# Kernel tuning notes

Hardware: AMD Instinct MI355X
Metric: run time of the kernel (lower is better)

## Reference

```python
import jax, jax.numpy as jnp
import numpy as np

N, E, C, NS, NB, NH = 20000, 320000, 64, 4, 8, 64
AVG_NEIGH = 16.0

def setup_inputs() -> dict:
    key = jax.random.key(0)
    ks = jax.random.split(key, 16)
    inp = {}
    inp['vectors'] = 0.35 * jax.random.normal(ks[0], (E, 3), jnp.float32)
    inp['node_scalars'] = jax.random.normal(ks[1], (N, C), jnp.float32)
    inp['node_vectors'] = jax.random.normal(ks[2], (N, C, 3), jnp.float32)
    inp['node_specie'] = jax.random.randint(ks[3], (N,), 0, NS)
    inp['senders'] = jax.random.randint(ks[4], (E,), 0, N)
    inp['receivers'] = jax.random.randint(ks[5], (E,), 0, N)
    # indexed skip linear: node irreps (64x0e+64x1o) -> 64x0e+64x1o+64x0e (scalars incl. gates)
    inp['W_skip_s'] = jax.random.normal(ks[6], (NS, C, 2 * C), jnp.float32) / np.sqrt(C)
    inp['W_skip_v'] = jax.random.normal(ks[7], (NS, C, C), jnp.float32) / np.sqrt(C)
    inp['W_up_s'] = jax.random.normal(ks[8], (C, C), jnp.float32) / np.sqrt(C)
    inp['W_up_v'] = jax.random.normal(ks[9], (C, C), jnp.float32) / np.sqrt(C)
    inp['W_mlp0'] = jax.random.normal(ks[10], (NB, NH), jnp.float32) / np.sqrt(NB)
    inp['W_mlp1'] = jax.random.normal(ks[11], (NH, NH), jnp.float32) / np.sqrt(NH)
    inp['W_mlp2'] = jax.random.normal(ks[12], (NH, 4 * C), jnp.float32) / np.sqrt(NH)
    inp['W_down_s'] = jax.random.normal(ks[13], (2 * C, 2 * C), jnp.float32) / np.sqrt(2 * C)
    inp['W_down_v'] = jax.random.normal(ks[14], (2 * C, C), jnp.float32) / np.sqrt(2 * C)
    return inp


def _forward(vectors, node_scalars, node_vectors, node_specie, senders, receivers,
             W_skip_s, W_skip_v, W_up_s, W_up_v, W_mlp0, W_mlp1, W_mlp2, W_down_s, W_down_v):
    n = node_scalars.shape[0]
    # --- self connection (specie-indexed linear) ---
    skip_s = jnp.einsum('ni,nio->no', node_scalars, W_skip_s[node_specie])   # [N,128]
    skip_v = jnp.einsum('nim,nio->nom', node_vectors, W_skip_v[node_specie]) # [N,64,3]
    # --- linear up ---
    s = node_scalars @ W_up_s                                  # [N,64]
    v = jnp.einsum('nim,io->nom', node_vectors, W_up_v)        # [N,64,3]
    ms, mv = s[senders], v[senders]                            # gather -> [E,64], [E,64,3]
    # --- spherical harmonics l=1, component normalization (|Y|=sqrt(3)) ---
    lengths = jnp.linalg.norm(vectors, axis=1, keepdims=True)  # [E,1]
    vhat = vectors / jnp.where(lengths == 0.0, 1.0, lengths)
    Y = jnp.sqrt(3.0) * vhat                                   # [E,3]
    # --- tensor product, filter_ir_out = {0e,1o} ---
    t1 = ms[:, :, None] * Y[:, None, :]                        # 0e x 1o -> 1o [E,64,3]
    t0 = jnp.einsum('ecm,em->ec', mv, Y) / jnp.sqrt(3.0)       # 1o x 1o -> 0e [E,64]
    msg_s = jnp.concatenate([ms, t0], axis=1)                  # [E,128]
    msg_v = jnp.concatenate([mv, t1], axis=1)                  # [E,128,3]
    # --- radial basis * polynomial envelope -> MLP ---
    x = lengths[:, 0]
    nvec = jnp.arange(1, NB + 1, dtype=vectors.dtype)
    safe_x = jnp.where(x == 0.0, 1.0, x)
    bess = jnp.sqrt(2.0) * jnp.sin(nvec * jnp.pi * x[:, None]) / safe_x[:, None]  # [E,8]
    u = jnp.clip(x, 0.0, 1.0)
    env = jnp.where(x < 1.0, 1.0 - 28.0 * u**6 + 48.0 * u**7 - 21.0 * u**8, 0.0)  # poly_envelope(5,2)
    h = jax.nn.swish((bess * env[:, None]) @ W_mlp0)
    h = jax.nn.swish(h @ W_mlp1)
    mix = h @ W_mlp2                                           # [E,256] = 128x0e + 128x1o weights
    mix = jnp.where(lengths == 0.0, 0.0, mix)
    msg_s = msg_s * mix[:, : 2 * C]
    msg_v = msg_v * mix[:, 2 * C :, None]
    # --- scatter-add to receivers, normalize by sqrt(avg_num_neighbors) ---
    inv = 1.0 / jnp.sqrt(AVG_NEIGH)
    agg_s = jnp.zeros((n, 2 * C), msg_s.dtype).at[receivers].add(msg_s) * inv
    agg_v = jnp.zeros((n, 2 * C, 3), msg_v.dtype).at[receivers].add(msg_v) * inv
    # --- linear down to 64x0e + 64x1o + 64x0e(gates) ---
    out_s = agg_s @ W_down_s + skip_s                          # [N,128]
    out_v = jnp.einsum('nim,io->nom', agg_v, W_down_v) + skip_v  # [N,64,3]
    # --- gate: swish on scalars, swish(gates) modulates vectors ---
    scal = jax.nn.swish(out_s[:, :C])
    gates = jax.nn.swish(out_s[:, C:])
    vec = out_v * gates[:, :, None]
    return jnp.concatenate([scal, vec.reshape(n, 3 * C)], axis=1)  # [N,256]


def reference(vectors, node_scalars, node_vectors, node_specie, senders, receivers,
              W_skip_s, W_skip_v, W_up_s, W_up_v, W_mlp0, W_mlp1, W_mlp2, W_down_s, W_down_v):
    return _forward(vectors, node_scalars, node_vectors, node_specie, senders, receivers,
                    W_skip_s, W_skip_v, W_up_s, W_up_v, W_mlp0, W_mlp1, W_mlp2, W_down_s, W_down_v)
```

## Files before the change

kernel.cpp:

```cpp
#include <hip/hip_runtime.h>
#include <math.h>

#define PI_F        3.14159265358979323846f
#define SQRT2_F     1.41421356237309515f
#define SQRT3_F     1.73205080756887729f
#define INV_SQRT3_F 0.57735026918962576f
#define INV_AVG     0.25f

#define N_NODES 20000
#define N_EDGES 320000

__device__ __forceinline__ float swish_f(float x) {
    return x / (1.f + __expf(-x));
}

__global__ __launch_bounds__(256) void k_zero_cnt(int* __restrict__ cnt) {
    const int i = blockIdx.x * 256 + threadIdx.x;
    if (i < N_NODES) cnt[i] = 0;
}
__global__ __launch_bounds__(256) void k_hist(const int* __restrict__ rcv,
                                              int* __restrict__ cnt) {
    const int e = blockIdx.x * 256 + threadIdx.x;
    if (e < N_EDGES) atomicAdd(&cnt[rcv[e]], 1);
}
__global__ __launch_bounds__(1024) void k_scan(const int* __restrict__ cnt,
                                               int* __restrict__ cursor) {
    __shared__ int part[1024];
    const int t = threadIdx.x;
    const int base = t * 20;
    int s = 0;
    #pragma unroll
    for (int j = 0; j < 20; ++j) {
        const int idx = base + j;
        if (idx < N_NODES) s += cnt[idx];
    }
    part[t] = s;
    __syncthreads();
    for (int d = 1; d < 1024; d <<= 1) {
        const int v = (t >= d) ? part[t - d] : 0;
        __syncthreads();
        part[t] += v;
        __syncthreads();
    }
    int run = (t == 0) ? 0 : part[t - 1];
    for (int j = 0; j < 20; ++j) {
        const int idx = base + j;
        if (idx < N_NODES) { cursor[idx] = run; run += cnt[idx]; }
    }
}
__global__ __launch_bounds__(256) void k_scatter(const int* __restrict__ rcv,
                                                 int* __restrict__ cursor,
                                                 int* __restrict__ perm) {
    const int e = blockIdx.x * 256 + threadIdx.x;
    if (e < N_EDGES) {
        const int pos = atomicAdd(&cursor[rcv[e]], 1);
        perm[pos] = e;
    }
}

__global__ __launch_bounds__(256) void k_node_up(
    const float* __restrict__ ns, const float* __restrict__ nv,
    const float* __restrict__ Wus, const float* __restrict__ Wuv,
    float* __restrict__ s_up, float* __restrict__ v_up,
    float* __restrict__ agg_s, float* __restrict__ agg_v)
{
    const int lane = threadIdx.x & 63;
    const int wq   = __builtin_amdgcn_readfirstlane(threadIdx.x >> 6);
    const int n    = blockIdx.x * 4 + wq;

    const float* nsr = ns + n * 64;
    const float* nvr = nv + n * 192;
    float acc = 0.f, a0 = 0.f, a1 = 0.f, a2 = 0.f;
    for (int i = 0; i < 64; ++i) {
        const float s = nsr[i];
        acc = fmaf(s, Wus[i*64 + lane], acc);
        const float wv = Wuv[i*64 + lane];
        a0 = fmaf(nvr[i*3+0], wv, a0);
        a1 = fmaf(nvr[i*3+1], wv, a1);
        a2 = fmaf(nvr[i*3+2], wv, a2);
    }
    s_up[n*64 + lane] = acc;
    v_up[(n*64 + lane)*3 + 0] = a0;
    v_up[(n*64 + lane)*3 + 1] = a1;
    v_up[(n*64 + lane)*3 + 2] = a2;

    agg_s[n*128 + lane]      = 0.f;
    agg_s[n*128 + 64 + lane] = 0.f;
    #pragma unroll
    for (int k = 0; k < 6; ++k) agg_v[n*384 + k*64 + lane] = 0.f;
}

__global__ __launch_bounds__(256, 4) void k_edge(
    const float* __restrict__ vecs,
    const int*   __restrict__ snd_idx, const int* __restrict__ rcv_idx,
    const int*   __restrict__ perm,
    const float* __restrict__ W0, const float* __restrict__ W1,
    const float* __restrict__ W2,
    const float* __restrict__ s_up, const float* __restrict__ v_up,
    float* __restrict__ agg_s, float* __restrict__ agg_v)
{
    __shared__ float h1v[64*69];
    __shared__ float h2v[64*69];

    const int tid  = threadIdx.x;
    const int lane = tid & 63;
    const int wq   = __builtin_amdgcn_readfirstlane(tid >> 6);
    const int e0   = blockIdx.x * 64;
    const int c    = lane & 15, q = lane >> 4;

    const int pe_l  = perm[e0 + lane];
    const int rcv_l = rcv_idx[pe_l];
    const int snd_l = snd_idx[pe_l];
    const float vx_l = vecs[pe_l*3+0], vy_l = vecs[pe_l*3+1], vz_l = vecs[pe_l*3+2];
    const float x_l  = sqrtf(vx_l*vx_l + vy_l*vy_l + vz_l*vz_l);
    const float sx_l = (x_l == 0.f) ? 1.f : x_l;
    const float ys_l = SQRT3_F / sx_l;
    const float Y0_l = vx_l * ys_l, Y1_l = vy_l * ys_l, Y2_l = vz_l * ys_l;
    const float msk_l = (x_l == 0.f) ? 0.f : 1.f;

    #pragma unroll 4
    for (int t = 0; t < 16; ++t) {
        const int le = wq*16 + t;
        const float x = __shfl(x_l, le);
        const float sx = (x == 0.f) ? 1.f : x;
        float s1, c1;
        __sincosf(PI_F * x, &s1, &c1);
        const float u  = fminf(x, 1.f);
        const float u2 = u*u, u3 = u2*u;
        const float u6 = u3*u3, u7 = u6*u, u8 = u6*u2;
        const float env  = (x < 1.f) ? (1.f - 28.f*u6 + 48.f*u7 - 21.f*u8) : 0.f;
        const float pref = SQRT2_F * env / sx;
        float h1 = 0.f;
        float sn = s1, snm1 = 0.f;
        const float twoc = 2.f * c1;
        #pragma unroll
        for (int b = 0; b < 8; ++b) {
            h1 = fmaf(pref * sn, W0[b*64 + lane], h1);
            const float snext = fmaf(twoc, sn, -snm1);
            snm1 = sn; sn = snext;
        }
        h1v[le*69 + lane] = swish_f(h1);
    }

    {
        float acc2[16];
        #pragma unroll
        for (int t = 0; t < 16; ++t) acc2[t] = 0.f;
        for (int i = 0; i < 64; ++i) {
            const float w = W1[i*64 + lane];
            #pragma unroll
            for (int t = 0; t < 16; ++t)
                acc2[t] = fmaf(h1v[(wq*16 + t)*69 + i], w, acc2[t]);
        }
        #pragma unroll
        for (int t = 0; t < 16; ++t)
            h2v[(wq*16 + t)*69 + lane] = swish_f(acc2[t]);
    }
    __syncthreads();

    float mixr[16][4];
    #pragma unroll
    for (int t = 0; t < 16; ++t)
        #pragma unroll
        for (int j = 0; j < 4; ++j) mixr[t][j] = 0.f;
    {
        const float* W2c = W2 + 64*wq + c;
        for (int i = 0; i < 64; ++i) {
            const float w0 = W2c[i*256 +  0];
            const float w1 = W2c[i*256 + 16];
            const float w2 = W2c[i*256 + 32];
            const float w3 = W2c[i*256 + 48];
            #pragma unroll
            for (int t = 0; t < 16; ++t) {
                const float h = h2v[(q*16 + t)*69 + i];
                mixr[t][0] = fmaf(h, w0, mixr[t][0]);
                mixr[t][1] = fmaf(h, w1, mixr[t][1]);
                mixr[t][2] = fmaf(h, w2, mixr[t][2]);
                mixr[t][3] = fmaf(h, w3, mixr[t][3]);
            }
        }
    }

    int cur = -1;
    if (wq == 0) {
        float ra0=0.f, ra1=0.f, ra2=0.f, ra3=0.f;
        #pragma unroll
        for (int t = 0; t < 16; ++t) {
            const int sl  = (lane & 48) + t;
            const int rcv = __shfl(rcv_l, sl);
            const int snd = __shfl(snd_l, sl);
            const float msk = __shfl(msk_l, sl);
            if (rcv != cur) {
                if (cur >= 0) {
                    float* p = agg_s + cur*128 + c;
                    unsafeAtomicAdd(p,      ra0);
                    unsafeAtomicAdd(p + 16, ra1);
                    unsafeAtomicAdd(p + 32, ra2);
                    unsafeAtomicAdd(p + 48, ra3);
                }
                ra0 = ra1 = ra2 = ra3 = 0.f; cur = rcv;
            }
            const float* sp = s_up + snd*64 + c;
            ra0 = fmaf(sp[0],  mixr[t][0] * msk, ra0);
            ra1 = fmaf(sp[16], mixr[t][1] * msk, ra1);
            ra2 = fmaf(sp[32], mixr[t][2] * msk, ra2);
            ra3 = fmaf(sp[48], mixr[t][3] * msk, ra3);
        }
        float* p = agg_s + cur*128 + c;
        unsafeAtomicAdd(p,      ra0);
        unsafeAtomicAdd(p + 16, ra1);
        unsafeAtomicAdd(p + 32, ra2);
        unsafeAtomicAdd(p + 48, ra3);
    } else if (wq == 1) {
        float ra0=0.f, ra1=0.f, ra2=0.f, ra3=0.f;
        #pragma unroll
        for (int t = 0; t < 16; ++t) {
            const int sl  = (lane & 48) + t;
            const int rcv = __shfl(rcv_l, sl);
            const int snd = __shfl(snd_l, sl);
            const float msk = __shfl(msk_l, sl);
            const float Y0 = __shfl(Y0_l, sl), Y1 = __shfl(Y1_l, sl), Y2 = __shfl(Y2_l, sl);
            if (rcv != cur) {
                if (cur >= 0) {
                    float* p = agg_s + cur*128 + 64 + c;
                    unsafeAtomicAdd(p,      ra0);
                    unsafeAtomicAdd(p + 16, ra1);
                    unsafeAtomicAdd(p + 32, ra2);
                    unsafeAtomicAdd(p + 48, ra3);
                }
                ra0 = ra1 = ra2 = ra3 = 0.f; cur = rcv;
            }
            const float* vp = v_up + (snd*64 + c)*3;
            const float t00 = (vp[  0]*Y0 + vp[  1]*Y1 + vp[  2]*Y2) * INV_SQRT3_F;
            const float t01 = (vp[ 48]*Y0 + vp[ 49]*Y1 + vp[ 50]*Y2) * INV_SQRT3_F;
            const float t02 = (vp[ 96]*Y0 + vp[ 97]*Y1 + vp[ 98]*Y2) * INV_SQRT3_F;
            const float t03 = (vp[144]*Y0 + vp[145]*Y1 + vp[146]*Y2) * INV_SQRT3_F;
            ra0 = fmaf(t00, mixr[t][0] * msk, ra0);
            ra1 = fmaf(t01, mixr[t][1] * msk, ra1);
            ra2 = fmaf(t02, mixr[t][2] * msk, ra2);
            ra3 = fmaf(t03, mixr[t][3] * msk, ra3);
        }
        float* p = agg_s + cur*128 + 64 + c;
        unsafeAtomicAdd(p,      ra0);
        unsafeAtomicAdd(p + 16, ra1);
        unsafeAtomicAdd(p + 32, ra2);
        unsafeAtomicAdd(p + 48, ra3);
    } else if (wq == 2) {
        float rv[4][3];
        #pragma unroll
        for (int i = 0; i < 4; ++i) { rv[i][0]=0.f; rv[i][1]=0.f; rv[i][2]=0.f; }
        #pragma unroll
        for (int t = 0; t < 16; ++t) {
            const int sl  = (lane & 48) + t;
            const int rcv = __shfl(rcv_l, sl);
            const int snd = __shfl(snd_l, sl);
            const float msk = __shfl(msk_l, sl);
            if (rcv != cur) {
                if (cur >= 0) {
                    float* p = agg_v + cur*384 + c*3;
                    #pragma unroll
                    for (int ntl = 0; ntl < 4; ++ntl)
                        #pragma unroll
                        for (int m = 0; m < 3; ++m)
                            unsafeAtomicAdd(p + ntl*48 + m, rv[ntl][m]);
                }
                #pragma unroll
                for (int i = 0; i < 4; ++i) { rv[i][0]=0.f; rv[i][1]=0.f; rv[i][2]=0.f; }
                cur = rcv;
            }
            const float* vp = v_up + (snd*64 + c)*3;
            #pragma unroll
            for (int ntl = 0; ntl < 4; ++ntl) {
                const float mx = mixr[t][ntl] * msk;
                #pragma unroll
                for (int m = 0; m < 3; ++m)
                    rv[ntl][m] = fmaf(vp[ntl*48 + m], mx, rv[ntl][m]);
            }
        }
        float* p = agg_v + cur*384 + c*3;
        #pragma unroll
        for (int ntl = 0; ntl < 4; ++ntl)
            #pragma unroll
            for (int m = 0; m < 3; ++m)
                unsafeAtomicAdd(p + ntl*48 + m, rv[ntl][m]);
    } else {
        float rv[4][3];
        #pragma unroll
        for (int i = 0; i < 4; ++i) { rv[i][0]=0.f; rv[i][1]=0.f; rv[i][2]=0.f; }
        #pragma unroll
        for (int t = 0; t < 16; ++t) {
            const int sl  = (lane & 48) + t;
            const int rcv = __shfl(rcv_l, sl);
            const int snd = __shfl(snd_l, sl);
            const float msk = __shfl(msk_l, sl);
            const float Y0 = __shfl(Y0_l, sl), Y1 = __shfl(Y1_l, sl), Y2 = __shfl(Y2_l, sl);
            if (rcv != cur) {
                if (cur >= 0) {
                    float* p = agg_v + cur*384 + 192 + c*3;
                    #pragma unroll
                    for (int ntl = 0; ntl < 4; ++ntl)
                        #pragma unroll
                        for (int m = 0; m < 3; ++m)
                            unsafeAtomicAdd(p + ntl*48 + m, rv[ntl][m]);
                }
                #pragma unroll
                for (int i = 0; i < 4; ++i) { rv[i][0]=0.f; rv[i][1]=0.f; rv[i][2]=0.f; }
                cur = rcv;
            }
            const float* sp = s_up + snd*64 + c;
            #pragma unroll
            for (int ntl = 0; ntl < 4; ++ntl) {
                const float mm = sp[ntl*16] * (mixr[t][ntl] * msk);
                rv[ntl][0] = fmaf(mm, Y0, rv[ntl][0]);
                rv[ntl][1] = fmaf(mm, Y1, rv[ntl][1]);
                rv[ntl][2] = fmaf(mm, Y2, rv[ntl][2]);
            }
        }
        float* p = agg_v + cur*384 + 192 + c*3;
        #pragma unroll
        for (int ntl = 0; ntl < 4; ++ntl)
            #pragma unroll
            for (int m = 0; m < 3; ++m)
                unsafeAtomicAdd(p + ntl*48 + m, rv[ntl][m]);
    }
}

__global__ __launch_bounds__(256) void k_node_down(
    const float* __restrict__ ns, const float* __restrict__ nv,
    const int*   __restrict__ spec_idx,
    const float* __restrict__ Wds, const float* __restrict__ Wdv,
    const float* __restrict__ Wsks, const float* __restrict__ Wskv,
    const float* __restrict__ agg_s, const float* __restrict__ agg_v,
    float* __restrict__ out)
{
    const int lane = threadIdx.x & 63;
    const int wq   = __builtin_amdgcn_readfirstlane(threadIdx.x >> 6);
    const int n    = blockIdx.x * 4 + wq;
    const int spec = __builtin_amdgcn_readfirstlane(spec_idx[n]);

    const float* ar  = agg_s + n*128;
    const float* avr = agg_v + n*384;
    float s0 = 0.f, s1 = 0.f, v0 = 0.f, v1 = 0.f, v2 = 0.f;
    for (int i = 0; i < 128; ++i) {
        const float a = ar[i] * INV_AVG;
        s0 = fmaf(a, Wds[i*128 + lane], s0);
        s1 = fmaf(a, Wds[i*128 + 64 + lane], s1);
        const float wv = Wdv[i*64 + lane];
        v0 = fmaf(avr[i*3+0] * INV_AVG, wv, v0);
        v1 = fmaf(avr[i*3+1] * INV_AVG, wv, v1);
        v2 = fmaf(avr[i*3+2] * INV_AVG, wv, v2);
    }
    const float* nsr = ns + n*64;
    const float* nvr = nv + n*192;
    const float* Ws  = Wsks + spec*8192;
    const float* Wv  = Wskv + spec*4096;
    for (int i = 0; i < 64; ++i) {
        const float s = nsr[i];
        s0 = fmaf(s, Ws[i*128 + lane], s0);
        s1 = fmaf(s, Ws[i*128 + 64 + lane], s1);
        const float wv = Wv[i*64 + lane];
        v0 = fmaf(nvr[i*3+0], wv, v0);
        v1 = fmaf(nvr[i*3+1], wv, v1);
        v2 = fmaf(nvr[i*3+2], wv, v2);
    }
    const float scal = swish_f(s0);
    const float gate = swish_f(s1);
    out[n*256 + lane]               = scal;
    out[n*256 + 64 + lane*3 + 0]    = v0 * gate;
    out[n*256 + 64 + lane*3 + 1]    = v1 * gate;
    out[n*256 + 64 + lane*3 + 2]    = v2 * gate;
}

extern "C" void kernel_launch(void* const* d_in, const int* in_sizes, int n_in,
                              void* d_out, int out_size, void* d_ws, size_t ws_size,
                              hipStream_t stream)
{
    (void)in_sizes; (void)n_in; (void)out_size; (void)ws_size;

    const float* vectors      = (const float*)d_in[0];
    const float* node_scalars = (const float*)d_in[1];
    const float* node_vectors = (const float*)d_in[2];
    const int*   node_specie  = (const int*)d_in[3];
    const int*   senders      = (const int*)d_in[4];
    const int*   receivers    = (const int*)d_in[5];
    const float* W_skip_s     = (const float*)d_in[6];
    const float* W_skip_v     = (const float*)d_in[7];
    const float* W_up_s       = (const float*)d_in[8];
    const float* W_up_v       = (const float*)d_in[9];
    const float* W_mlp0       = (const float*)d_in[10];
    const float* W_mlp1       = (const float*)d_in[11];
    const float* W_mlp2       = (const float*)d_in[12];
    const float* W_down_s     = (const float*)d_in[13];
    const float* W_down_v     = (const float*)d_in[14];
    float* out = (float*)d_out;

    float* ws    = (float*)d_ws;
    float* s_up  = ws;
    float* v_up  = s_up + 1280000;
    float* agg_s = v_up + 3840000;
    float* agg_v = agg_s + 2560000;
    int*   perm  = (int*)(agg_v + 7680000);
    int*   cnt    = (int*)agg_s;
    int*   cursor = cnt + 20000;

    hipLaunchKernelGGL(k_zero_cnt, dim3(79),   dim3(256),  0, stream, cnt);
    hipLaunchKernelGGL(k_hist,     dim3(1250), dim3(256),  0, stream, receivers, cnt);
    hipLaunchKernelGGL(k_scan,     dim3(1),    dim3(1024), 0, stream, cnt, cursor);
    hipLaunchKernelGGL(k_scatter,  dim3(1250), dim3(256),  0, stream, receivers, cursor, perm);

    hipLaunchKernelGGL(k_node_up, dim3(5000), dim3(256), 0, stream,
        node_scalars, node_vectors, W_up_s, W_up_v, s_up, v_up, agg_s, agg_v);
    hipLaunchKernelGGL(k_edge, dim3(5000), dim3(256), 0, stream,
        vectors, senders, receivers, perm, W_mlp0, W_mlp1, W_mlp2,
        s_up, v_up, agg_s, agg_v);
    hipLaunchKernelGGL(k_node_down, dim3(5000), dim3(256), 0, stream,
        node_scalars, node_vectors, node_specie, W_down_s, W_down_v,
        W_skip_s, W_skip_v, agg_s, agg_v, out);
}
```

Measured before the change: 539.8 us.

## Transpose edge MLP hidden buffers and use packed FMA with vector LDS reads

The two padded LDS buffers for the edge MLP hidden layers become one transposed buffer laid out [feature][edge], stride 68, shared by both layers. Each thread now reads four consecutive edges' activations with a single 128-bit LDS load. The accumulators become float2 vectors so the compiler can emit packed FMA (v_pk_fma_f32) in the two MLP matmul loops, cutting LDS instruction count and VALU issue slots. Reusing one buffer halves LDS footprint, but the h1 write must now wait until each wave finishes its own reads, and the stride-68 layout may cause bank conflicts.

```diff
diff --git a/kernel.cpp b/kernel.cpp
--- a/kernel.cpp
+++ b/kernel.cpp
@@ -9,6 +9,9 @@
 
 #define N_NODES 20000
 #define N_EDGES 320000
+
+typedef float v2f __attribute__((ext_vector_type(2)));
+typedef float v4f __attribute__((ext_vector_type(4)));
 
 __device__ __forceinline__ float swish_f(float x) {
     return x / (1.f + __expf(-x));
@@ -99,8 +102,7 @@
     const float* __restrict__ s_up, const float* __restrict__ v_up,
     float* __restrict__ agg_s, float* __restrict__ agg_v)
 {
-    __shared__ float h1v[64*69];
-    __shared__ float h2v[64*69];
+    __shared__ float hv[64*68];
 
     const int tid  = threadIdx.x;
     const int lane = tid & 63;
@@ -118,6 +120,7 @@
     const float Y0_l = vx_l * ys_l, Y1_l = vy_l * ys_l, Y2_l = vz_l * ys_l;
     const float msk_l = (x_l == 0.f) ? 0.f : 1.f;
 
+    float h1o[16];
     #pragma unroll 4
     for (int t = 0; t < 16; ++t) {
         const int le = wq*16 + t;
@@ -139,47 +142,73 @@
             const float snext = fmaf(twoc, sn, -snm1);
             snm1 = sn; sn = snext;
         }
-        h1v[le*69 + lane] = swish_f(h1);
-    }
-
+        h1o[t] = swish_f(h1);
+    }
     {
-        float acc2[16];
-        #pragma unroll
-        for (int t = 0; t < 16; ++t) acc2[t] = 0.f;
+        float* dst = hv + lane*68 + wq*16;
+        #pragma unroll
+        for (int k = 0; k < 4; ++k)
+            ((v4f*)dst)[k] = (v4f){h1o[4*k], h1o[4*k+1], h1o[4*k+2], h1o[4*k+3]};
+    }
+
+    {
+        v2f acc2[8];
+        #pragma unroll
+        for (int tp = 0; tp < 8; ++tp) acc2[tp] = (v2f){0.f, 0.f};
+        const float* hbase = hv + wq*16;
         for (int i = 0; i < 64; ++i) {
             const float w = W1[i*64 + lane];
-            #pragma unroll
-            for (int t = 0; t < 16; ++t)
-                acc2[t] = fmaf(h1v[(wq*16 + t)*69 + i], w, acc2[t]);
-        }
-        #pragma unroll
-        for (int t = 0; t < 16; ++t)
-            h2v[(wq*16 + t)*69 + lane] = swish_f(acc2[t]);
+            const v2f wv = {w, w};
+            const v4f* hp4 = (const v4f*)(hbase + i*68);
+            #pragma unroll
+            for (int k = 0; k < 4; ++k) {
+                const v4f h4 = hp4[k];
+                const v2f hlo = __builtin_shufflevector(h4, h4, 0, 1);
+                const v2f hhi = __builtin_shufflevector(h4, h4, 2, 3);
+                acc2[2*k]   = __builtin_elementwise_fma(hlo, wv, acc2[2*k]);
+                acc2[2*k+1] = __builtin_elementwise_fma(hhi, wv, acc2[2*k+1]);
+            }
+        }
+        float* dst = hv + lane*68 + wq*16;
+        #pragma unroll
+        for (int k = 0; k < 4; ++k)
+            ((v4f*)dst)[k] = (v4f){swish_f(acc2[2*k][0]),   swish_f(acc2[2*k][1]),
+                                   swish_f(acc2[2*k+1][0]), swish_f(acc2[2*k+1][1])};
     }
     __syncthreads();
 
-    float mixr[16][4];
+    v2f mixp[8][4];
     #pragma unroll
-    for (int t = 0; t < 16; ++t)
-        #pragma unroll
-        for (int j = 0; j < 4; ++j) mixr[t][j] = 0.f;
+    for (int tp = 0; tp < 8; ++tp)
+        #pragma unroll
+        for (int j = 0; j < 4; ++j) mixp[tp][j] = (v2f){0.f, 0.f};
     {
         const float* W2c = W2 + 64*wq + c;
+        const float* hq  = hv + q*16;
         for (int i = 0; i < 64; ++i) {
             const float w0 = W2c[i*256 +  0];
             const float w1 = W2c[i*256 + 16];
             const float w2 = W2c[i*256 + 32];
             const float w3 = W2c[i*256 + 48];
-            #pragma unroll
-            for (int t = 0; t < 16; ++t) {
-                const float h = h2v[(q*16 + t)*69 + i];
-                mixr[t][0] = fmaf(h, w0, mixr[t][0]);
-                mixr[t][1] = fmaf(h, w1, mixr[t][1]);
-                mixr[t][2] = fmaf(h, w2, mixr[t][2]);
-                mixr[t][3] = fmaf(h, w3, mixr[t][3]);
-            }
-        }
-    }
+            const v2f w0v = {w0,w0}, w1v = {w1,w1}, w2v = {w2,w2}, w3v = {w3,w3};
+            const v4f* hp4 = (const v4f*)(hq + i*68);
+            #pragma unroll
+            for (int k = 0; k < 4; ++k) {
+                const v4f h4 = hp4[k];
+                const v2f hlo = __builtin_shufflevector(h4, h4, 0, 1);
+                const v2f hhi = __builtin_shufflevector(h4, h4, 2, 3);
+                mixp[2*k][0]   = __builtin_elementwise_fma(hlo, w0v, mixp[2*k][0]);
+                mixp[2*k][1]   = __builtin_elementwise_fma(hlo, w1v, mixp[2*k][1]);
+                mixp[2*k][2]   = __builtin_elementwise_fma(hlo, w2v, mixp[2*k][2]);
+                mixp[2*k][3]   = __builtin_elementwise_fma(hlo, w3v, mixp[2*k][3]);
+                mixp[2*k+1][0] = __builtin_elementwise_fma(hhi, w0v, mixp[2*k+1][0]);
+                mixp[2*k+1][1] = __builtin_elementwise_fma(hhi, w1v, mixp[2*k+1][1]);
+                mixp[2*k+1][2] = __builtin_elementwise_fma(hhi, w2v, mixp[2*k+1][2]);
+                mixp[2*k+1][3] = __builtin_elementwise_fma(hhi, w3v, mixp[2*k+1][3]);
+            }
+        }
+    }
+    #define MIXR(t,j) (mixp[(t)>>1][j][(t)&1])
 
     int cur = -1;
     if (wq == 0) {
@@ -201,10 +230,10 @@
                 ra0 = ra1 = ra2 = ra3 = 0.f; cur = rcv;
             }
             const float* sp = s_up + snd*64 + c;
-            ra0 = fmaf(sp[0],  mixr[t][0] * msk, ra0);
-            ra1 = fmaf(sp[16], mixr[t][1] * msk, ra1);
-            ra2 = fmaf(sp[32], mixr[t][2] * msk, ra2);
-            ra3 = fmaf(sp[48], mixr[t][3] * msk, ra3);
+            ra0 = fmaf(sp[0],  MIXR(t,0) * msk, ra0);
+            ra1 = fmaf(sp[16], MIXR(t,1) * msk, ra1);
+            ra2 = fmaf(sp[32], MIXR(t,2) * msk, ra2);
+            ra3 = fmaf(sp[48], MIXR(t,3) * msk, ra3);
         }
         float* p = agg_s + cur*128 + c;
         unsafeAtomicAdd(p,      ra0);
@@ -235,10 +264,10 @@
             const float t01 = (vp[ 48]*Y0 + vp[ 49]*Y1 + vp[ 50]*Y2) * INV_SQRT3_F;
             const float t02 = (vp[ 96]*Y0 + vp[ 97]*Y1 + vp[ 98]*Y2) * INV_SQRT3_F;
             const float t03 = (vp[144]*Y0 + vp[145]*Y1 + vp[146]*Y2) * INV_SQRT3_F;
-            ra0 = fmaf(t00, mixr[t][0] * msk, ra0);
-            ra1 = fmaf(t01, mixr[t][1] * msk, ra1);
-            ra2 = fmaf(t02, mixr[t][2] * msk, ra2);
-            ra3 = fmaf(t03, mixr[t][3] * msk, ra3);
+            ra0 = fmaf(t00, MIXR(t,0) * msk, ra0);
+            ra1 = fmaf(t01, MIXR(t,1) * msk, ra1);
+            ra2 = fmaf(t02, MIXR(t,2) * msk, ra2);
+            ra3 = fmaf(t03, MIXR(t,3) * msk, ra3);
         }
         float* p = agg_s + cur*128 + 64 + c;
         unsafeAtomicAdd(p,      ra0);
@@ -271,7 +300,7 @@
             const float* vp = v_up + (snd*64 + c)*3;
             #pragma unroll
             for (int ntl = 0; ntl < 4; ++ntl) {
-                const float mx = mixr[t][ntl] * msk;
+                const float mx = MIXR(t,ntl) * msk;
                 #pragma unroll
                 for (int m = 0; m < 3; ++m)
                     rv[ntl][m] = fmaf(vp[ntl*48 + m], mx, rv[ntl][m]);
@@ -310,7 +339,7 @@
             const float* sp = s_up + snd*64 + c;
             #pragma unroll
             for (int ntl = 0; ntl < 4; ++ntl) {
-                const float mm = sp[ntl*16] * (mixr[t][ntl] * msk);
+                const float mm = sp[ntl*16] * (MIXR(t,ntl) * msk);
                 rv[ntl][0] = fmaf(mm, Y0, rv[ntl][0]);
                 rv[ntl][1] = fmaf(mm, Y1, rv[ntl][1]);
                 rv[ntl][2] = fmaf(mm, Y2, rv[ntl][2]);
@@ -323,6 +352,7 @@
             for (int m = 0; m < 3; ++m)
                 unsafeAtomicAdd(p + ntl*48 + m, rv[ntl][m]);
     }
+    #undef MIXR
 }
 
 __global__ __launch_bounds__(256) void k_node_down(
```

Result: faster. 529.1 us (-2.0%).
